# Kernel optimization log

Hardware: AMD Instinct MI355X
Metric: run time of the kernel (lower is better)

The kernel has to match this reference:

```python
import jax, jax.numpy as jnp
import numpy as np

BN_EPS = 1e-5

def knn_idx(x, k):
    # x: [bs, C, N] -> idx [bs, N, k] of k nearest neighbors in feature space (incl. self)
    xx = jnp.sum(x * x, axis=1)                      # [bs, N]
    inner = jnp.einsum('bcn,bcm->bnm', x, x)         # [bs, N, N]
    neg_dist = 2.0 * inner - xx[:, :, None] - xx[:, None, :]
    _, idx = jax.lax.top_k(neg_dist, k)
    return idx

def gcn_encoder(x, k, W, b, gamma, beta):
    # DGCNN-style EdgeConv: x [bs, C, N] -> [bs, O, N]
    idx = knn_idx(x, k)                              # [bs, N, k]
    xt = jnp.transpose(x, (0, 2, 1))                 # [bs, N, C]
    nb = jax.vmap(lambda f, i: f[i])(xt, idx)        # [bs, N, k, C] neighbor gather
    center = jnp.broadcast_to(xt[:, :, None, :], nb.shape)
    edge = jnp.concatenate([nb - center, center], axis=-1)   # [bs, N, k, 2C]
    h = jnp.einsum('bnkc,oc->bnko', edge, W) + b             # 1x1 conv
    # BatchNorm (eval, running_mean=0, running_var=1)
    h = gamma * h * (1.0 / jnp.sqrt(1.0 + BN_EPS)) + beta
    h = jax.nn.relu(h)
    h = jnp.max(h, axis=2)                           # max over k neighbors -> [bs, N, O]
    return jnp.transpose(h, (0, 2, 1))               # [bs, O, N]

def setup_inputs() -> dict:
    key = jax.random.key(0)
    ks = jax.random.split(key, 6)
    bs, cin, n_stk, n_pnt = 8, 128, 32, 128
    cu, cout = 2 * cin, 256
    scale = 1.0 / np.sqrt(2 * cu)
    return {
        'sparse_fea': jax.random.normal(ks[0], (bs, cin, n_stk), jnp.float32),
        'dense_fea': jax.random.normal(ks[1], (bs, cin, n_stk, n_pnt), jnp.float32),
        'W_sp': jax.random.normal(ks[2], (cout, 2 * cu), jnp.float32) * scale,
        'b_sp': jnp.zeros((cout,), jnp.float32),
        'g_sp': jnp.ones((cout,), jnp.float32),
        'be_sp': jnp.zeros((cout,), jnp.float32),
        'W_dn': jax.random.normal(ks[3], (cout, 2 * cu), jnp.float32) * scale,
        'b_dn': jnp.zeros((cout,), jnp.float32),
        'g_dn': jnp.ones((cout,), jnp.float32),
        'be_dn': jnp.zeros((cout,), jnp.float32),
        'W_conv': jax.random.normal(ks[4], (cout, cout, 1, 3), jnp.float32) * (1.0 / np.sqrt(3 * cout)),
        'b_conv': jnp.zeros((cout,), jnp.float32),
        'g_c': jnp.ones((cout,), jnp.float32),
        'be_c': jnp.zeros((cout,), jnp.float32),
    }

def reference(sparse_fea, dense_fea, W_sp, b_sp, g_sp, be_sp,
              W_dn, b_dn, g_dn, be_dn, W_conv, b_conv, g_c, be_c):
    # DenseToSparse: max over points + concat channels
    u_sp = jnp.concatenate([sparse_fea, jnp.max(dense_fea, axis=3)], axis=1)   # [bs, 2C, n_stk]
    # SparseToDense: broadcast sparse over points + concat channels
    bs, C, n_stk, n_pnt = dense_fea.shape
    sp_bcast = jnp.broadcast_to(sparse_fea[..., None], (bs, C, n_stk, n_pnt))
    u_dn = jnp.concatenate([dense_fea, sp_bcast], axis=1)                      # [bs, 2C, n_stk, n_pnt]
    # SparseUpdate: kNN GCN over strokes, k=2
    u_sp = gcn_encoder(u_sp, 2, W_sp, b_sp, g_sp, be_sp)                       # [bs, O, n_stk]
    # DenseUpdate: flatten points, kNN GCN, k=10
    flat = u_dn.reshape(bs, 2 * C, n_stk * n_pnt)
    flat = gcn_encoder(flat, 10, W_dn, b_dn, g_dn, be_dn)                      # [bs, O, N]
    u_dn = flat.reshape(bs, flat.shape[1], n_stk, n_pnt)
    # DownSample: Conv2d k=(1,3) s=(1,2) p=(0,1) + BN(eval) + ReLU (Dropout2d: eval identity)
    y = jax.lax.conv_general_dilated(u_dn, W_conv, window_strides=(1, 2),
                                     padding=((0, 0), (1, 1)),
                                     dimension_numbers=('NCHW', 'OIHW', 'NCHW'))
    y = y + b_conv[None, :, None, None]
    y = g_c[None, :, None, None] * y * (1.0 / jnp.sqrt(1.0 + BN_EPS)) + be_c[None, :, None, None]
    y = jax.nn.relu(y)
    return (u_sp, y)
```

## Files before the change

kernel.cpp:

```cpp
#include <hip/hip_runtime.h>

using s16x8 = __attribute__((ext_vector_type(8))) short;
using f32x4 = __attribute__((ext_vector_type(4))) float;

#define MFMA(a, b, c) __builtin_amdgcn_mfma_f32_16x16x32_bf16((a), (b), (c), 0, 0, 0)
#define INVBN 0.9999950000374997f

__device__ __forceinline__ float b2f(unsigned short u) {
    return __uint_as_float(((unsigned int)u) << 16);
}
__device__ __forceinline__ unsigned short f2b(float f) {
    unsigned int x = __float_as_uint(f);
    unsigned int r = x + 0x7FFFu + ((x >> 16) & 1u);
    return (unsigned short)(r >> 16);
}
__device__ __forceinline__ unsigned umin_(unsigned a, unsigned b) { return a < b ? a : b; }
__device__ __forceinline__ unsigned umax_(unsigned a, unsigned b) { return a > b ? a : b; }
#define CE(a, b) { unsigned lo_ = umin_(a, b), hi_ = umax_(a, b); (a) = lo_; (b) = hi_; }

#define BITONIC_RESORT16(v) { \
    _Pragma("unroll") for (int i_ = 0; i_ < 8; i_++) CE(v[i_], v[i_ + 8]) \
    _Pragma("unroll") for (int g_ = 0; g_ < 2; g_++) \
    _Pragma("unroll") for (int i_ = 0; i_ < 4; i_++) CE(v[g_ * 8 + i_], v[g_ * 8 + i_ + 4]) \
    _Pragma("unroll") for (int g_ = 0; g_ < 4; g_++) \
    _Pragma("unroll") for (int i_ = 0; i_ < 2; i_++) CE(v[g_ * 4 + i_], v[g_ * 4 + i_ + 2]) \
    _Pragma("unroll") for (int g_ = 0; g_ < 8; g_++) CE(v[g_ * 2], v[g_ * 2 + 1]) }

#define SORT8_MERGE(c8, v) { \
    CE(c8[0], c8[1]) CE(c8[2], c8[3]) CE(c8[4], c8[5]) CE(c8[6], c8[7]) \
    CE(c8[0], c8[2]) CE(c8[1], c8[3]) CE(c8[4], c8[6]) CE(c8[5], c8[7]) \
    CE(c8[1], c8[2]) CE(c8[5], c8[6]) \
    CE(c8[0], c8[4]) CE(c8[1], c8[5]) CE(c8[2], c8[6]) CE(c8[3], c8[7]) \
    CE(c8[2], c8[4]) CE(c8[3], c8[5]) \
    CE(c8[1], c8[2]) CE(c8[3], c8[4]) CE(c8[5], c8[6]) \
    _Pragma("unroll") for (int i_ = 0; i_ < 8; i_++) v[i_] = umax_(v[i_], c8[7 - i_]); \
    BITONIC_RESORT16(v) }

#define XLANE_MERGE(v) { \
    _Pragma("unroll") for (int lev_ = 0; lev_ < 2; lev_++) { \
        int m_ = lev_ == 0 ? 16 : 32; \
        unsigned o_[16]; \
        _Pragma("unroll") for (int i_ = 0; i_ < 16; i_++) \
            o_[i_] = (unsigned)__shfl_xor((int)v[15 - i_], m_, 64); \
        _Pragma("unroll") for (int i_ = 0; i_ < 16; i_++) v[i_] = umax_(v[i_], o_[i_]); \
        BITONIC_RESORT16(v) } }

__global__ __launch_bounds__(256) void k_sparse_u0(const float* sp, const float* dn,
                                                   float* usp0, float* xxsp) {
    int s = blockIdx.x, b = blockIdx.y, c = threadIdx.x;
    float v;
    if (c < 128) {
        v = sp[(b * 128 + c) * 32 + s];
    } else {
        const float* row = dn + ((size_t)((b * 128 + (c - 128)) * 32 + s)) * 128;
        float m = -3.0e38f;
        for (int p = 0; p < 128; p++) m = fmaxf(m, row[p]);
        v = m;
    }
    usp0[(size_t)(b * 32 + s) * 256 + c] = v;
    __shared__ float red[256];
    red[c] = v * v;
    __syncthreads();
    for (int st = 128; st > 0; st >>= 1) {
        if (c < st) red[c] += red[c + st];
        __syncthreads();
    }
    if (c == 0) xxsp[b * 32 + s] = red[0];
}

__global__ __launch_bounds__(64) void k_sparse_knn(const float* usp0, const float* xxsp, int* idxsp) {
    int n = blockIdx.x, b = blockIdx.y, t = threadIdx.x;
    float nd = -3.0e38f;
    if (t < 32) {
        const float* xn = usp0 + (size_t)(b * 32 + n) * 256;
        const float* xj = usp0 + (size_t)(b * 32 + t) * 256;
        float inner = 0.f;
        for (int c = 0; c < 256; c++) inner += xn[c] * xj[c];
        nd = 2.f * inner - xxsp[b * 32 + n] - xxsp[b * 32 + t];
    }
    float best1 = -3.0e38f, best2 = -3.0e38f;
    int i1 = 0, i2 = 0;
    for (int jj = 0; jj < 32; jj++) {
        float vv = __shfl(nd, jj, 64);
        if (vv > best1) { best2 = best1; i2 = i1; best1 = vv; i1 = jj; }
        else if (vv > best2) { best2 = vv; i2 = jj; }
    }
    if (t == 0) {
        idxsp[(b * 32 + n) * 2] = i1;
        idxsp[(b * 32 + n) * 2 + 1] = i2;
    }
}

__global__ __launch_bounds__(256) void k_sparse_edge(const float* usp0, const int* idxsp,
                                                     const float* wsp, const float* bsp,
                                                     const float* gsp, const float* besp,
                                                     float* out) {
    int n = blockIdx.x, b = blockIdx.y, t = threadIdx.x;
    __shared__ float ctr[256], nb0[256], nb1[256];
    int i0 = idxsp[(b * 32 + n) * 2], i1 = idxsp[(b * 32 + n) * 2 + 1];
    ctr[t] = usp0[(size_t)(b * 32 + n) * 256 + t];
    nb0[t] = usp0[(size_t)(b * 32 + i0) * 256 + t];
    nb1[t] = usp0[(size_t)(b * 32 + i1) * 256 + t];
    __syncthreads();
    const float* wrow = wsp + (size_t)t * 512;
    float a0 = 0.f, a1 = 0.f, ac = 0.f;
    for (int c = 0; c < 256; c++) {
        float w1 = wrow[c], w2 = wrow[256 + c];
        float cc = ctr[c];
        a0 += (nb0[c] - cc) * w1;
        a1 += (nb1[c] - cc) * w1;
        ac += cc * w2;
    }
    float g = gsp[t], bb = bsp[t], be = besp[t];
    float h0 = g * INVBN * (a0 + ac + bb) + be;
    float h1 = g * INVBN * (a1 + ac + bb) + be;
    out[((size_t)(b * 256 + t)) * 32 + n] = fmaxf(fmaxf(h0, h1), 0.f);
}

__global__ __launch_bounds__(256) void k_build_xdn(const float* sp, const float* dn,
                                                   unsigned short* xdn, float* xdnf) {
    int bx = blockIdx.x;
    int s = bx >> 2, q = bx & 3;
    int b = blockIdx.y, t = threadIdx.x;
    __shared__ float tile[32 * 131];
    float spv = 0.f;
    if (t >= 128) spv = sp[(b * 128 + (t - 128)) * 32 + s];
    int pl = t & 31, ch = t >> 5;
#pragma unroll
    for (int it = 0; it < 16; it++) {
        int c = it * 8 + ch;
        tile[pl * 131 + c] = dn[((size_t)((b * 128 + c) * 32 + s)) * 128 + q * 32 + pl];
    }
    __syncthreads();
    for (int pp = 0; pp < 32; pp++) {
        float v = (t < 128) ? tile[pp * 131 + t] : spv;
        size_t row = (size_t)(b * 4096) + s * 128 + q * 32 + pp;
        xdnf[row * 256 + t] = v;
        xdn[row * 256 + t] = f2b(v);
    }
}

__global__ __launch_bounds__(256) void k_xx(const float* xdnf, float* xx, double* xxd) {
    int b = blockIdx.y;
    int w = threadIdx.x >> 6, l = threadIdx.x & 63;
    int n = blockIdx.x * 4 + w;
    const float* row = xdnf + ((size_t)b * 4096 + n) * 256;
    f32x4 v = *(const f32x4*)(row + l * 4);
    double s = 0.0;
#pragma unroll
    for (int i = 0; i < 4; i++) s += (double)v[i] * v[i];
#pragma unroll
    for (int off = 32; off > 0; off >>= 1) s += __shfl_down(s, off, 64);
    if (l == 0) {
        xx[(size_t)b * 4096 + n] = (float)s;
        xxd[(size_t)b * 4096 + n] = s;
    }
}

__global__ __launch_bounds__(256) void k_wcat(const float* wdn, unsigned short* wcat) {
    int j = blockIdx.x, c = threadIdx.x;
    if (j < 256) {
        wcat[j * 256 + c] = f2b(wdn[j * 512 + c]);
    } else {
        int o = j - 256;
        wcat[j * 256 + c] = f2b(wdn[o * 512 + 256 + c] - wdn[o * 512 + c]);
    }
}

__global__ __launch_bounds__(512, 4) void k_dense_knn(const unsigned short* xdn, const float* xx, int* cand) {
    int b = blockIdx.y;
    int rb = blockIdx.x >> 1;
    int h = blockIdx.x & 1;
    int r0 = rb * 128;
    int c0base = h * 2048;
    int t = threadIdx.x;
    int g = t >> 8;
    int tg = t & 255;
    int wr = (t >> 6) & 3;
    int l = t & 63;
    __shared__ __align__(16) char smem_raw[2 * 32 * 264 * 2 + 256];
    unsigned short* acol = (unsigned short*)smem_raw;
    float* xxc = (float*)(smem_raw + 2 * 32 * 264 * 2);
    unsigned* g1k = (unsigned*)smem_raw;
    size_t bN = (size_t)b * 4096;
    int row0 = wr * 32 + (l & 15);
    int row1 = row0 + 16;

    unsigned short* acolg = acol + g * (32 * 264);

    s16x8 bfrag0[8], bfrag1[8];
    {
        const s16x8* gb0 = (const s16x8*)(xdn + (bN + r0 + row0) * 256 + (l >> 4) * 8);
        const s16x8* gb1 = (const s16x8*)(xdn + (bN + r0 + row1) * 256 + (l >> 4) * 8);
#pragma unroll
        for (int ks = 0; ks < 8; ks++) { bfrag0[ks] = gb0[ks * 4]; bfrag1[ks] = gb1[ks * 4]; }
    }

    unsigned v16a[16], v16b[16];
#pragma unroll
    for (int i = 0; i < 16; i++) { v16a[i] = 0u; v16b[i] = 0u; }

    for (int ct = 0; ct < 32; ct++) {
        int c0 = c0base + (ct * 2 + g) * 32;
        __syncthreads();
        {
            int r = tg & 31, seg = tg >> 5;
            const s16x8* src = (const s16x8*)(xdn + (bN + c0 + r) * 256 + seg * 32);
            s16x8* dst = (s16x8*)(acolg + r * 264 + seg * 32);
#pragma unroll
            for (int u = 0; u < 4; u++) dst[u] = src[u];
        }
        if (tg < 32) xxc[g * 32 + tg] = xx[bN + c0 + tg];
        __syncthreads();
        f32x4 a00 = {0.f, 0.f, 0.f, 0.f}, a01 = {0.f, 0.f, 0.f, 0.f};
        f32x4 a10 = {0.f, 0.f, 0.f, 0.f}, a11 = {0.f, 0.f, 0.f, 0.f};
        const unsigned short* ap0 = acolg + (l & 15) * 264 + (l >> 4) * 8;
        const unsigned short* ap1 = ap0 + 16 * 264;
#pragma unroll
        for (int ks = 0; ks < 8; ks++) {
            s16x8 ca = *(const s16x8*)(ap0 + ks * 32);
            s16x8 cb = *(const s16x8*)(ap1 + ks * 32);
            a00 = MFMA(ca, bfrag0[ks], a00);
            a01 = MFMA(cb, bfrag0[ks], a01);
            a10 = MFMA(ca, bfrag1[ks], a10);
            a11 = MFMA(cb, bfrag1[ks], a11);
        }
        {
            unsigned c8[8];
#pragma unroll
            for (int j = 0; j < 4; j++) {
                int cl0 = (l >> 4) * 4 + j;
                float d0 = 2.f * a00[j] - xxc[g * 32 + cl0];
                unsigned u0 = __float_as_uint(d0);
                u0 ^= ((unsigned)((int)u0 >> 31)) | 0x80000000u;
                c8[j] = (u0 & 0xFFFFF000u) | (unsigned)(c0 + cl0);
                int cl1 = cl0 + 16;
                float d1 = 2.f * a01[j] - xxc[g * 32 + cl1];
                unsigned u1 = __float_as_uint(d1);
                u1 ^= ((unsigned)((int)u1 >> 31)) | 0x80000000u;
                c8[4 + j] = (u1 & 0xFFFFF000u) | (unsigned)(c0 + cl1);
            }
            SORT8_MERGE(c8, v16a)
        }
        {
            unsigned c8[8];
#pragma unroll
            for (int j = 0; j < 4; j++) {
                int cl0 = (l >> 4) * 4 + j;
                float d0 = 2.f * a10[j] - xxc[g * 32 + cl0];
                unsigned u0 = __float_as_uint(d0);
                u0 ^= ((unsigned)((int)u0 >> 31)) | 0x80000000u;
                c8[j] = (u0 & 0xFFFFF000u) | (unsigned)(c0 + cl0);
                int cl1 = cl0 + 16;
                float d1 = 2.f * a11[j] - xxc[g * 32 + cl1];
                unsigned u1 = __float_as_uint(d1);
                u1 ^= ((unsigned)((int)u1 >> 31)) | 0x80000000u;
                c8[4 + j] = (u1 & 0xFFFFF000u) | (unsigned)(c0 + cl1);
            }
            SORT8_MERGE(c8, v16b)
        }
    }

    XLANE_MERGE(v16a)
    XLANE_MERGE(v16b)

    __syncthreads();
    if (g == 1 && (l >> 4) == 0) {
#pragma unroll
        for (int i = 0; i < 16; i++) {
            g1k[row0 * 16 + i] = v16a[i];
            g1k[row1 * 16 + i] = v16b[i];
        }
    }
    __syncthreads();
    if (g == 0 && (l >> 4) == 0) {
        {
            unsigned o[16];
#pragma unroll
            for (int i = 0; i < 16; i++) o[i] = g1k[row0 * 16 + 15 - i];
#pragma unroll
            for (int i = 0; i < 16; i++) v16a[i] = umax_(v16a[i], o[i]);
            BITONIC_RESORT16(v16a)
            int* dst = cand + (bN + r0 + row0) * 32 + h * 16;
#pragma unroll
            for (int i = 0; i < 16; i++) dst[i] = (int)(v16a[i] & 0xFFFu);
        }
        {
            unsigned o[16];
#pragma unroll
            for (int i = 0; i < 16; i++) o[i] = g1k[row1 * 16 + 15 - i];
#pragma unroll
            for (int i = 0; i < 16; i++) v16b[i] = umax_(v16b[i], o[i]);
            BITONIC_RESORT16(v16b)
            int* dst = cand + (bN + r0 + row1) * 32 + h * 16;
#pragma unroll
            for (int i = 0; i < 16; i++) dst[i] = (int)(v16b[i] & 0xFFFu);
        }
    }
}

__global__ __launch_bounds__(256) void k_rerank(const float* xdnf, const double* xxd,
                                                const int* cand, int* idxdn) {
    int flat = blockIdx.x;
    int b = flat & 7;
    int n0 = (flat >> 3) * 8;
    int t = threadIdx.x;
    int r = t >> 5;
    int qg = (t >> 2) & 7;
    int chunk = t & 3;
    __shared__ float xa[8][260];
    __shared__ double dred[8][32];
    __shared__ double xxdn[8];
    __shared__ int cidx[8][32];
    size_t bN = (size_t)b * 4096;
    {
        int rr = t >> 5, qq = t & 31;
        const float* src = xdnf + (bN + n0 + rr) * 256 + qq * 8;
        *(f32x4*)&xa[rr][qq * 8] = *(const f32x4*)src;
        *(f32x4*)&xa[rr][qq * 8 + 4] = *(const f32x4*)(src + 4);
        if (t < 8) xxdn[t] = xxd[bN + n0 + t];
        cidx[rr][qq] = cand[(bN + n0 + rr) * 32 + qq];
    }
    __syncthreads();
#pragma unroll
    for (int p = 0; p < 4; p++) {
        int q = p * 8 + qg;
        int j = cidx[r][q];
        const float* xb = xdnf + (bN + j) * 256 + chunk * 4;
        const float* xav = &xa[r][chunk * 4];
        double ac0 = 0.0, ac1 = 0.0, ac2 = 0.0, ac3 = 0.0;
#pragma unroll 8
        for (int c4 = 0; c4 < 16; c4++) {
            f32x4 a = *(const f32x4*)(xav + c4 * 16);
            f32x4 bb = *(const f32x4*)(xb + c4 * 16);
            ac0 += (double)a[0] * bb[0];
            ac1 += (double)a[1] * bb[1];
            ac2 += (double)a[2] * bb[2];
            ac3 += (double)a[3] * bb[3];
        }
        double acc = (ac0 + ac1) + (ac2 + ac3);
        acc += __shfl_xor(acc, 1, 64);
        acc += __shfl_xor(acc, 2, 64);
        if (chunk == 0)
            dred[r][q] = 2.0 * acc - xxdn[r] - xxd[bN + j];
    }
    __syncthreads();
    if (t < 8) {
        int used = 0;
        int* dst = idxdn + (bN + n0 + t) * 10;
        for (int rank = 0; rank < 10; rank++) {
            double best = -1.0e300;
            int bi = 0;
#pragma unroll
            for (int i = 0; i < 32; i++) {
                bool ok = !((used >> i) & 1) && dred[t][i] > best;
                if (ok) { best = dred[t][i]; bi = i; }
            }
            used |= (1 << bi);
            dst[rank] = cidx[t][bi];
        }
    }
}

__global__ __launch_bounds__(256) void k_pq_gemm(const unsigned short* xdn, const unsigned short* wcat,
                                                 unsigned short* cpq) {
    int j0 = blockIdx.x * 64;
    int n0 = blockIdx.y * 64;
    int b = blockIdx.z;
    int t = threadIdx.x, w = t >> 6, l = t & 63;
    __shared__ __align__(16) unsigned short arow[64 * 264];
    __shared__ __align__(16) unsigned short brow[32 * 264];
    __shared__ float outb[64 * 34];
    {
        int r = t >> 2, seg = t & 3;
        const unsigned short* src = xdn + ((size_t)b * 4096 + n0 + r) * 256 + seg * 64;
        unsigned short* dst = arow + r * 264 + seg * 64;
#pragma unroll
        for (int u = 0; u < 8; u++) *(s16x8*)(dst + 8 * u) = *(const s16x8*)(src + 8 * u);
    }
    {
        int r = t >> 3, seg = t & 7;
        const unsigned short* src = wcat + (size_t)(j0 + r) * 256 + seg * 32;
        unsigned short* dst = brow + r * 264 + seg * 32;
#pragma unroll
        for (int u = 0; u < 4; u++) *(s16x8*)(dst + 8 * u) = *(const s16x8*)(src + 8 * u);
    }
    __syncthreads();
    const unsigned short* ap = arow + (w * 16 + (l & 15)) * 264 + (l >> 4) * 8;
    const unsigned short* bp0 = brow + (l & 15) * 264 + (l >> 4) * 8;
    const unsigned short* bp1 = brow + (16 + (l & 15)) * 264 + (l >> 4) * 8;
#pragma unroll
    for (int jt = 0; jt < 2; jt++) {
        f32x4 acc0 = {0.f, 0.f, 0.f, 0.f}, acc1 = {0.f, 0.f, 0.f, 0.f};
#pragma unroll
        for (int ks = 0; ks < 8; ks++) {
            s16x8 af = *(const s16x8*)(ap + ks * 32);
            acc0 = MFMA(af, *(const s16x8*)(bp0 + ks * 32), acc0);
            acc1 = MFMA(af, *(const s16x8*)(bp1 + ks * 32), acc1);
        }
        __syncthreads();
        if (jt == 0) {
            int r = t >> 3, seg = t & 7;
            const unsigned short* src = wcat + (size_t)(j0 + 32 + r) * 256 + seg * 32;
            unsigned short* dst = brow + r * 264 + seg * 32;
#pragma unroll
            for (int u = 0; u < 4; u++) *(s16x8*)(dst + 8 * u) = *(const s16x8*)(src + 8 * u);
        }
#pragma unroll
        for (int j = 0; j < 4; j++) {
            int row = w * 16 + (l >> 4) * 4 + j;
            outb[row * 34 + (l & 15)] = acc0[j];
            outb[row * 34 + 16 + (l & 15)] = acc1[j];
        }
        __syncthreads();
#pragma unroll
        for (int it = 0; it < 8; it++) {
            int r = it * 8 + (t >> 5);
            int c = t & 31;
            cpq[((size_t)b * 4096 + n0 + r) * 512 + j0 + jt * 32 + c] = f2b(outb[r * 34 + c]);
        }
    }
}

__global__ void k_pad_zero(unsigned short* upad) {
    int s = blockIdx.x, b = blockIdx.y, t = threadIdx.x;
    size_t base = ((size_t)(b * 32 + s)) * 130 * 256;
    upad[base + t] = 0;
    upad[base + 129 * 256 + t] = 0;
}

__global__ __launch_bounds__(256) void k_combine(const unsigned short* cpq, const int* idxdn,
                                                 const float* bdn, const float* gdn,
                                                 const float* bedn, unsigned short* upad) {
    int flat = blockIdx.x;
    int b = flat & 7;
    int n = flat >> 3;
    int s = n >> 7, p = n & 127;
    int t = threadIdx.x;
    const int* ix = idxdn + ((size_t)b * 4096 + n) * 10;
    float qv = b2f(cpq[((size_t)b * 4096 + n) * 512 + 256 + t]);
    float g = gdn[t], bb = bdn[t], be = bedn[t];
    float a = g * INVBN;
    float d = a * (qv + bb) + be;
    float m = -3.0e38f;
#pragma unroll
    for (int kk = 0; kk < 10; kk++) {
        int j = ix[kk];
        float pv = b2f(cpq[((size_t)b * 4096 + j) * 512 + t]);
        m = fmaxf(m, a * pv + d);
    }
    upad[(((size_t)(b * 32 + s)) * 130 + 1 + p) * 256 + t] = f2b(fmaxf(m, 0.f));
}

__global__ void k_wconv_r(const float* wcv, unsigned short* wr) {
    int o = blockIdx.x, c = threadIdx.x;
#pragma unroll
    for (int i = 0; i < 3; i++) wr[o * 768 + i * 256 + c] = f2b(wcv[o * 768 + c * 3 + i]);
}

__global__ __launch_bounds__(256) void k_conv(const unsigned short* upad, const unsigned short* wr,
                                              const float* bcv, const float* gc,
                                              const float* bec, float* out) {
    int j0 = blockIdx.x * 64;
    int mb = blockIdx.y;
    int b = mb >> 5, s = mb & 31;
    int t = threadIdx.x, w = t >> 6, l = t & 63;
    __shared__ __align__(16) unsigned short at[64 * 72];
    __shared__ __align__(16) unsigned short bt[64 * 72];
    __shared__ float outb[64 * 66];
    f32x4 acc[4];
#pragma unroll
    for (int i = 0; i < 4; i++) acc[i] = (f32x4){0.f, 0.f, 0.f, 0.f};
    const size_t abase = ((size_t)(b * 32 + s)) * 130 * 256;
    for (int kc = 0; kc < 12; kc++) {
        __syncthreads();
        {
            int r = t >> 2, seg = t & 3;
            const unsigned short* src = upad + abase + (size_t)(2 * r) * 256 + kc * 64 + seg * 16;
            unsigned short* dst = at + r * 72 + seg * 16;
            *(s16x8*)dst = *(const s16x8*)src;
            *(s16x8*)(dst + 8) = *(const s16x8*)(src + 8);
            const unsigned short* src2 = wr + (size_t)(j0 + r) * 768 + kc * 64 + seg * 16;
            unsigned short* dst2 = bt + r * 72 + seg * 16;
            *(s16x8*)dst2 = *(const s16x8*)src2;
            *(s16x8*)(dst2 + 8) = *(const s16x8*)(src2 + 8);
        }
        __syncthreads();
#pragma unroll
        for (int ks = 0; ks < 2; ks++) {
            s16x8 af = *(const s16x8*)(at + (w * 16 + (l & 15)) * 72 + ks * 32 + (l >> 4) * 8);
#pragma unroll
            for (int cs = 0; cs < 4; cs++) {
                s16x8 bf = *(const s16x8*)(bt + (cs * 16 + (l & 15)) * 72 + ks * 32 + (l >> 4) * 8);
                acc[cs] = MFMA(af, bf, acc[cs]);
            }
        }
    }
    __syncthreads();
#pragma unroll
    for (int cs = 0; cs < 4; cs++)
#pragma unroll
        for (int j = 0; j < 4; j++)
            outb[(w * 16 + (l >> 4) * 4 + j) * 66 + cs * 16 + (l & 15)] = acc[cs][j];
    __syncthreads();
#pragma unroll
    for (int it = 0; it < 16; it++) {
        int oo = it * 4 + (t >> 6);
        int q = t & 63;
        int o = j0 + oo;
        float v = outb[q * 66 + oo];
        float y = fmaxf(gc[o] * INVBN * (v + bcv[o]) + bec[o], 0.f);
        out[65536 + (((size_t)(b * 256 + o)) * 32 + s) * 64 + q] = y;
    }
}

extern "C" void kernel_launch(void* const* d_in, const int* in_sizes, int n_in,
                              void* d_out, int out_size, void* d_ws, size_t ws_size,
                              hipStream_t stream) {
    const float* sp = (const float*)d_in[0];
    const float* dn = (const float*)d_in[1];
    const float* Wsp = (const float*)d_in[2];
    const float* bsp = (const float*)d_in[3];
    const float* gsp = (const float*)d_in[4];
    const float* besp = (const float*)d_in[5];
    const float* Wdn = (const float*)d_in[6];
    const float* bdn = (const float*)d_in[7];
    const float* gdn = (const float*)d_in[8];
    const float* bedn = (const float*)d_in[9];
    const float* Wcv = (const float*)d_in[10];
    const float* bcv = (const float*)d_in[11];
    const float* gc = (const float*)d_in[12];
    const float* bec = (const float*)d_in[13];
    float* out = (float*)d_out;
    char* ws = (char*)d_ws;

    size_t o_xdn = 0;
    size_t o_xdnf = o_xdn + 16777216;
    size_t o_cpq = o_xdnf + 33554432;
    size_t o_upad = o_cpq + 33554432;
    size_t o_wcat = o_upad + 17039360;
    size_t o_wr = o_wcat + 262144;
    size_t o_xx = o_wr + 393216;
    size_t o_xxd = o_xx + 131072;
    size_t o_cand = o_xxd + 262144;
    size_t o_idx = o_cand + 4194304;
    size_t o_usp0 = o_idx + 1310720;
    size_t o_xxsp = o_usp0 + 262144;
    size_t o_idxsp = o_xxsp + 1024;

    unsigned short* xdn = (unsigned short*)(ws + o_xdn);
    float* xdnf = (float*)(ws + o_xdnf);
    unsigned short* cpq = (unsigned short*)(ws + o_cpq);
    unsigned short* upad = (unsigned short*)(ws + o_upad);
    unsigned short* wcat = (unsigned short*)(ws + o_wcat);
    unsigned short* wr = (unsigned short*)(ws + o_wr);
    float* xx = (float*)(ws + o_xx);
    double* xxd = (double*)(ws + o_xxd);
    int* cand = (int*)(ws + o_cand);
    int* idxdn = (int*)(ws + o_idx);
    float* usp0 = (float*)(ws + o_usp0);
    float* xxsp = (float*)(ws + o_xxsp);
    int* idxsp = (int*)(ws + o_idxsp);

    k_sparse_u0<<<dim3(32, 8), 256, 0, stream>>>(sp, dn, usp0, xxsp);
    k_sparse_knn<<<dim3(32, 8), 64, 0, stream>>>(usp0, xxsp, idxsp);
    k_sparse_edge<<<dim3(32, 8), 256, 0, stream>>>(usp0, idxsp, Wsp, bsp, gsp, besp, out);

    k_build_xdn<<<dim3(128, 8), 256, 0, stream>>>(sp, dn, xdn, xdnf);
    k_xx<<<dim3(1024, 8), 256, 0, stream>>>(xdnf, xx, xxd);
    k_wcat<<<dim3(512), 256, 0, stream>>>(Wdn, wcat);
    k_dense_knn<<<dim3(64, 8), 512, 0, stream>>>(xdn, xx, cand);
    k_rerank<<<dim3(4096), 256, 0, stream>>>(xdnf, xxd, cand, idxdn);
    k_pq_gemm<<<dim3(8, 64, 8), 256, 0, stream>>>(xdn, wcat, cpq);
    k_pad_zero<<<dim3(32, 8), 256, 0, stream>>>(upad);
    k_combine<<<dim3(32768), 256, 0, stream>>>(cpq, idxdn, bdn, gdn, bedn, upad);

    k_wconv_r<<<dim3(256), 256, 0, stream>>>(Wcv, wr);
    k_conv<<<dim3(4, 256), 256, 0, stream>>>(upad, wr, bcv, gc, bec, out);
}
```

Before: 378.4 us.

## Fuse xx norms into build_xdn, prefetch kNN column tiles, fold pad zeroing

```diff
diff --git a/kernel.cpp b/kernel.cpp
--- a/kernel.cpp
+++ b/kernel.cpp
@@ -118,11 +118,14 @@
 }
 
 __global__ __launch_bounds__(256) void k_build_xdn(const float* sp, const float* dn,
-                                                   unsigned short* xdn, float* xdnf) {
+                                                   unsigned short* xdn, float* xdnf,
+                                                   float* xx, double* xxd) {
     int bx = blockIdx.x;
     int s = bx >> 2, q = bx & 3;
     int b = blockIdx.y, t = threadIdx.x;
     __shared__ float tile[32 * 131];
+    __shared__ double spred[128];
+    __shared__ double spsum_sh;
     float spv = 0.f;
     if (t >= 128) spv = sp[(b * 128 + (t - 128)) * 32 + s];
     int pl = t & 31, ch = t >> 5;
@@ -131,29 +134,37 @@
         int c = it * 8 + ch;
         tile[pl * 131 + c] = dn[((size_t)((b * 128 + c) * 32 + s)) * 128 + q * 32 + pl];
     }
-    __syncthreads();
+    if (t >= 128) spred[t - 128] = (double)spv * spv;
+    __syncthreads();
+    if (t == 0) {
+        double ssum = 0.0;
+        for (int i = 0; i < 128; i++) ssum += spred[i];
+        spsum_sh = ssum;
+    }
     for (int pp = 0; pp < 32; pp++) {
         float v = (t < 128) ? tile[pp * 131 + t] : spv;
         size_t row = (size_t)(b * 4096) + s * 128 + q * 32 + pp;
         xdnf[row * 256 + t] = v;
         xdn[row * 256 + t] = f2b(v);
     }
-}
-
-__global__ __launch_bounds__(256) void k_xx(const float* xdnf, float* xx, double* xxd) {
-    int b = blockIdx.y;
-    int w = threadIdx.x >> 6, l = threadIdx.x & 63;
-    int n = blockIdx.x * 4 + w;
-    const float* row = xdnf + ((size_t)b * 4096 + n) * 256;
-    f32x4 v = *(const f32x4*)(row + l * 4);
-    double s = 0.0;
-#pragma unroll
-    for (int i = 0; i < 4; i++) s += (double)v[i] * v[i];
-#pragma unroll
-    for (int off = 32; off > 0; off >>= 1) s += __shfl_down(s, off, 64);
-    if (l == 0) {
-        xx[(size_t)b * 4096 + n] = (float)s;
-        xxd[(size_t)b * 4096 + n] = s;
+    __syncthreads();
+    {
+        int pp = t >> 3, seg = t & 7;
+        double ps = 0.0;
+#pragma unroll
+        for (int i = 0; i < 16; i++) {
+            float v = tile[pp * 131 + seg * 16 + i];
+            ps += (double)v * v;
+        }
+        ps += __shfl_xor(ps, 1, 64);
+        ps += __shfl_xor(ps, 2, 64);
+        ps += __shfl_xor(ps, 4, 64);
+        if (seg == 0) {
+            double tot = ps + spsum_sh;
+            size_t row = (size_t)(b * 4096) + s * 128 + q * 32 + pp;
+            xx[row] = (float)tot;
+            xxd[row] = tot;
+        }
     }
 }
 
@@ -187,6 +198,7 @@
     int row1 = row0 + 16;
 
     unsigned short* acolg = acol + g * (32 * 264);
+    int sr = tg & 31, sseg = tg >> 5;
 
     s16x8 bfrag0[8], bfrag1[8];
     {
@@ -196,6 +208,16 @@
         for (int ks = 0; ks < 8; ks++) { bfrag0[ks] = gb0[ks * 4]; bfrag1[ks] = gb1[ks * 4]; }
     }
 
+    s16x8 stg[4];
+    float xxstg = 0.f;
+    {
+        int c0 = c0base + g * 32;
+        const s16x8* src = (const s16x8*)(xdn + (bN + c0 + sr) * 256 + sseg * 32);
+#pragma unroll
+        for (int u = 0; u < 4; u++) stg[u] = src[u];
+        if (tg < 32) xxstg = xx[bN + c0 + tg];
+    }
+
     unsigned v16a[16], v16b[16];
 #pragma unroll
     for (int i = 0; i < 16; i++) { v16a[i] = 0u; v16b[i] = 0u; }
@@ -204,13 +226,18 @@
         int c0 = c0base + (ct * 2 + g) * 32;
         __syncthreads();
         {
-            int r = tg & 31, seg = tg >> 5;
-            const s16x8* src = (const s16x8*)(xdn + (bN + c0 + r) * 256 + seg * 32);
-            s16x8* dst = (s16x8*)(acolg + r * 264 + seg * 32);
-#pragma unroll
-            for (int u = 0; u < 4; u++) dst[u] = src[u];
-        }
-        if (tg < 32) xxc[g * 32 + tg] = xx[bN + c0 + tg];
+            s16x8* dst = (s16x8*)(acolg + sr * 264 + sseg * 32);
+#pragma unroll
+            for (int u = 0; u < 4; u++) dst[u] = stg[u];
+        }
+        if (tg < 32) xxc[g * 32 + tg] = xxstg;
+        if (ct < 31) {
+            int c0n = c0base + ((ct + 1) * 2 + g) * 32;
+            const s16x8* src = (const s16x8*)(xdn + (bN + c0n + sr) * 256 + sseg * 32);
+#pragma unroll
+            for (int u = 0; u < 4; u++) stg[u] = src[u];
+            if (tg < 32) xxstg = xx[bN + c0n + tg];
+        }
         __syncthreads();
         f32x4 a00 = {0.f, 0.f, 0.f, 0.f}, a01 = {0.f, 0.f, 0.f, 0.f};
         f32x4 a10 = {0.f, 0.f, 0.f, 0.f}, a11 = {0.f, 0.f, 0.f, 0.f};
@@ -422,13 +449,6 @@
     }
 }
 
-__global__ void k_pad_zero(unsigned short* upad) {
-    int s = blockIdx.x, b = blockIdx.y, t = threadIdx.x;
-    size_t base = ((size_t)(b * 32 + s)) * 130 * 256;
-    upad[base + t] = 0;
-    upad[base + 129 * 256 + t] = 0;
-}
-
 __global__ __launch_bounds__(256) void k_combine(const unsigned short* cpq, const int* idxdn,
                                                  const float* bdn, const float* gdn,
                                                  const float* bedn, unsigned short* upad) {
@@ -449,7 +469,10 @@
         float pv = b2f(cpq[((size_t)b * 4096 + j) * 512 + t]);
         m = fmaxf(m, a * pv + d);
     }
-    upad[(((size_t)(b * 32 + s)) * 130 + 1 + p) * 256 + t] = f2b(fmaxf(m, 0.f));
+    size_t sb = ((size_t)(b * 32 + s)) * 130;
+    upad[(sb + 1 + p) * 256 + t] = f2b(fmaxf(m, 0.f));
+    if (p == 0) upad[sb * 256 + t] = 0;
+    if (p == 127) upad[(sb + 129) * 256 + t] = 0;
 }
 
 __global__ void k_wconv_r(const float* wcv, unsigned short* wr) {
@@ -566,13 +589,11 @@
     k_sparse_knn<<<dim3(32, 8), 64, 0, stream>>>(usp0, xxsp, idxsp);
     k_sparse_edge<<<dim3(32, 8), 256, 0, stream>>>(usp0, idxsp, Wsp, bsp, gsp, besp, out);
 
-    k_build_xdn<<<dim3(128, 8), 256, 0, stream>>>(sp, dn, xdn, xdnf);
-    k_xx<<<dim3(1024, 8), 256, 0, stream>>>(xdnf, xx, xxd);
+    k_build_xdn<<<dim3(128, 8), 256, 0, stream>>>(sp, dn, xdn, xdnf, xx, xxd);
     k_wcat<<<dim3(512), 256, 0, stream>>>(Wdn, wcat);
     k_dense_knn<<<dim3(64, 8), 512, 0, stream>>>(xdn, xx, cand);
     k_rerank<<<dim3(4096), 256, 0, stream>>>(xdnf, xxd, cand, idxdn);
     k_pq_gemm<<<dim3(8, 64, 8), 256, 0, stream>>>(xdn, wcat, cpq);
-    k_pad_zero<<<dim3(32, 8), 256, 0, stream>>>(upad);
     k_combine<<<dim3(32768), 256, 0, stream>>>(cpq, idxdn, bdn, gdn, bedn, upad);
 
     k_wconv_r<<<dim3(256), 256, 0, stream>>>(Wcv, wr);
```

After: 671.0 us. +77.3%, slower.
